# Optimization experiments

Hardware: AMD Instinct MI355X
Metric: run time of the kernel (lower is better)

Reference implementation:

```python
import jax, jax.numpy as jnp
import numpy as np

N_H, N_O, D = 5000, 15000, 1024
E_HH, E_OO, E_HO = 20000, 40000, 40000


def setup_inputs() -> dict:
    key = jax.random.key(0)
    ks = jax.random.split(key, 20)
    N = N_H + N_O
    w = lambda k, shp: jax.random.normal(k, shp, dtype=jnp.float32) * 0.02
    inp = {
        'n_f': jax.random.normal(ks[0], (N, D), dtype=jnp.float32),
        'src_hh': jax.random.randint(ks[1], (E_HH,), 0, N_H),
        'dst_hh': jax.random.randint(ks[2], (E_HH,), 0, N_H),
        'src_oo': jax.random.randint(ks[3], (E_OO,), 0, N_O) + N_H,
        'dst_oo': jax.random.randint(ks[4], (E_OO,), 0, N_O) + N_H,
        'src_ho': jax.random.randint(ks[5], (E_HO,), 0, N_H),
        'dst_ho': jax.random.randint(ks[6], (E_HO,), 0, N_O) + N_H,
        'W_hh': w(ks[7], (2 * D, D)), 'b_hh': jnp.zeros((D,), jnp.float32),
        'W_oo': w(ks[8], (2 * D, D)), 'b_oo': jnp.zeros((D,), jnp.float32),
        'W_ho': w(ks[9], (2 * D, D)), 'b_ho': jnp.zeros((D,), jnp.float32),
        'W_att': w(ks[10], (D, 1)), 'b_att': jnp.zeros((1,), jnp.float32),
        'W_hn': w(ks[11], (2 * D, D)), 'b_hn': jnp.zeros((D,), jnp.float32),
        'W_on': w(ks[12], (2 * D, D)), 'b_on': jnp.zeros((D,), jnp.float32),
    }
    return inp


def reference(n_f, src_hh, dst_hh, src_oo, dst_oo, src_ho, dst_ho,
              W_hh, b_hh, W_oo, b_oo, W_ho, b_ho, W_att, b_att,
              W_hn, b_hn, W_on, b_on):
    N = n_f.shape[0]

    def edge_mlp(src, dst, W, b):
        # gather -> concat -> Linear -> ReLU  (H_H/O_O/H_O EdgeApplyModule)
        feat = jnp.concatenate([n_f[src], n_f[dst]], axis=1)  # [E, 2D]
        return jax.nn.relu(feat @ W + b)                       # [E, D]

    e_f = jnp.concatenate([
        edge_mlp(src_hh, dst_hh, W_hh, b_hh),
        edge_mlp(src_oo, dst_oo, W_oo, b_oo),
        edge_mlp(src_ho, dst_ho, W_ho, b_ho),
    ], axis=0)                                                 # [E, D]
    src = jnp.concatenate([src_hh, src_oo, src_ho])
    dst = jnp.concatenate([dst_hh, dst_oo, dst_ho])

    # E_AttentionModule: per-edge scalar attention logit
    a = (e_f @ W_att + b_att)[:, 0]                            # [E]

    # update_all: per-destination softmax over incoming edges (mailbox softmax)
    seg_max = jax.ops.segment_max(a, dst, num_segments=N)
    seg_max = jnp.where(jnp.isfinite(seg_max), seg_max, 0.0)
    ex = jnp.exp(a - seg_max[dst])
    denom = jax.ops.segment_sum(ex, dst, num_segments=N)
    alpha = ex / jnp.where(denom[dst] == 0, 1.0, denom[dst])   # [E]
    z = jax.ops.segment_sum(alpha[:, None] * n_f[src], dst, num_segments=N)  # [N, D]

    # Node apply: concat(n_f, z_f) -> Linear -> ReLU, separate h/o MLPs
    new_h = jax.nn.relu(jnp.concatenate([n_f[:N_H], z[:N_H]], axis=1) @ W_hn + b_hn)
    new_o = jax.nn.relu(jnp.concatenate([n_f[N_H:], z[N_H:]], axis=1) @ W_on + b_on)
    return jnp.concatenate([new_h, new_o], axis=0)             # [N, D] new_n_f
```

## Files before the change

### kernel.cpp

```cpp
#include <hip/hip_runtime.h>

#define N_H   5000
#define N_O   15000
#define N_TOT 20000
#define DD    1024
#define E_HH  20000
#define E_OO  40000
#define E_HO  40000
#define E_TOT 100000

typedef unsigned short u16;
typedef unsigned int u32;
typedef __attribute__((ext_vector_type(8))) short short8;
typedef __attribute__((ext_vector_type(4))) float f32x4;
typedef const __attribute__((address_space(1))) u32 gas_u32;
typedef __attribute__((address_space(3))) u32 las_u32;

__device__ __forceinline__ float bf2f(u16 u) {
    union { unsigned int i; float f; } v; v.i = ((unsigned int)u) << 16; return v.f;
}
__device__ __forceinline__ u16 f2bf(float f) {
    union { float f; unsigned int i; } v; v.f = f;
    unsigned int u = v.i;
    return (u16)((u + 0x7FFFu + ((u >> 16) & 1u)) >> 16);
}

#define CAST_NB 10000
__global__ void cast_cat(const float* __restrict__ in, u16* __restrict__ out,
                         const int* __restrict__ shh, const int* __restrict__ dhh,
                         const int* __restrict__ soo, const int* __restrict__ doo,
                         const int* __restrict__ sho, const int* __restrict__ dho,
                         int* __restrict__ src_all, int* __restrict__ dst_all,
                         int* __restrict__ deg) {
    int b = blockIdx.x;
    if (b < CAST_NB) {
        size_t i = ((size_t)b * 256 + threadIdx.x) * 8;
        float4 a = *(const float4*)(in + i);
        float4 c = *(const float4*)(in + i + 4);
        u16 o[8] = {f2bf(a.x), f2bf(a.y), f2bf(a.z), f2bf(a.w),
                    f2bf(c.x), f2bf(c.y), f2bf(c.z), f2bf(c.w)};
        *(uint4*)(out + i) = *(const uint4*)o;
        return;
    }
    int e = (b - CAST_NB) * 256 + threadIdx.x;
    if (e >= E_TOT) return;
    int s, d;
    if (e < E_HH)              { s = shh[e];               d = dhh[e]; }
    else if (e < E_HH + E_OO)  { s = soo[e - E_HH];        d = doo[e - E_HH]; }
    else                       { s = sho[e - E_HH - E_OO]; d = dho[e - E_HH - E_OO]; }
    src_all[e] = s; dst_all[e] = d;
    atomicAdd(&deg[d], 1);
}

struct TW  { const float* W; u16* dT; u16* dB; int ld; };
struct TW5 { TW t[5]; };
__global__ void transpose_all(TW5 p) {
    __shared__ float tile[32][33];
    int z = blockIdx.z;
    TW tw = p.t[z >> 1];
    int half = z & 1;
    int bk = blockIdx.x, bn = blockIdx.y;
    int tx = threadIdx.x & 31, ty = threadIdx.x >> 5;
#pragma unroll
    for (int yy = 0; yy < 4; yy++) {
        int k = half * 1024 + bk * 32 + ty + yy * 8;
        int n = bn * 32 + tx;
        tile[ty + yy * 8][tx] = tw.W[(size_t)k * 1024 + n];
    }
    __syncthreads();
    u16* dst = half ? tw.dB : tw.dT;
#pragma unroll
    for (int yy = 0; yy < 4; yy++) {
        int n = bn * 32 + ty + yy * 8;
        int k = bk * 32 + tx;
        dst[(size_t)n * tw.ld + k] = f2bf(tile[tx][ty + yy * 8]);
    }
}

#define PROJ_NBM_H 40
#define PROJ_NBM_O 118
#define PROJ_NBN   24
__launch_bounds__(256)
__global__ void gemm_proj(const u16* __restrict__ Ah, const u16* __restrict__ Ao,
                          const u16* __restrict__ Bth, const u16* __restrict__ Bto,
                          u16* __restrict__ Ch, u16* __restrict__ Co) {
    __shared__ u16 smem[2][128][64];
    int bid = blockIdx.x;
    const u16* A; const u16* Bt; u16* C; int M;
    if (bid < PROJ_NBM_H * PROJ_NBN) { A = Ah; Bt = Bth; C = Ch; M = N_H; }
    else { bid -= PROJ_NBM_H * PROJ_NBN; A = Ao; Bt = Bto; C = Co; M = N_O; }
    int bm = bid / PROJ_NBN, bn = bid % PROJ_NBN;
    int t = threadIdx.x;
    int wave = t >> 6, lane = t & 63;
    int wr = wave >> 1, wc = wave & 1;
    int lm = lane & 15, q = lane >> 4;
    f32x4 acc[4][4] = {};
    int srow = lane >> 3;
    int scol = ((lane & 7) ^ srow) * 8;

    for (int k0 = 0; k0 < 1024; k0 += 64) {
#pragma unroll
        for (int it = 0; it < 4; it++) {
            int chunk = wave * 4 + it;
            int row = chunk * 8 + srow;
            int gr = bm * 128 + row; if (gr >= M) gr = M - 1;
            __builtin_amdgcn_global_load_lds((gas_u32*)(A + (size_t)gr * 1024 + k0 + scol),
                                             (las_u32*)&smem[0][chunk * 8][0], 16, 0, 0);
            __builtin_amdgcn_global_load_lds((gas_u32*)(Bt + (size_t)(bn * 128 + row) * 1024 + k0 + scol),
                                             (las_u32*)&smem[1][chunk * 8][0], 16, 0, 0);
        }
        __syncthreads();
#pragma unroll
        for (int ks = 0; ks < 64; ks += 32) {
            short8 af[4], bfr[4];
            int pc = (((ks >> 3) + q) ^ (lm & 7)) * 8;
#pragma unroll
            for (int i = 0; i < 4; i++)
                af[i] = *(const short8*)&smem[0][wr * 64 + i * 16 + lm][pc];
#pragma unroll
            for (int j = 0; j < 4; j++)
                bfr[j] = *(const short8*)&smem[1][wc * 64 + j * 16 + lm][pc];
#pragma unroll
            for (int i = 0; i < 4; i++)
#pragma unroll
                for (int j = 0; j < 4; j++)
                    acc[i][j] = __builtin_amdgcn_mfma_f32_16x16x32_bf16(af[i], bfr[j], acc[i][j], 0, 0, 0);
        }
        __syncthreads();
    }
    u16* sc = &smem[0][0][0];
#pragma unroll
    for (int i = 0; i < 4; i++)
#pragma unroll
        for (int j = 0; j < 4; j++)
#pragma unroll
            for (int r = 0; r < 4; r++)
                sc[(wr * 64 + i * 16 + q * 4 + r) * 128 + (wc * 64 + j * 16 + lm)] =
                    f2bf(acc[i][j][r]);
    __syncthreads();
#pragma unroll
    for (int it = 0; it < 8; it++) {
        int flat = it * 256 + t;
        int r = flat >> 4, cs = (flat & 15) * 8;
        int grow = bm * 128 + r;
        if (grow < M)
            *(uint4*)&C[(size_t)grow * 3072 + bn * 128 + cs] = *(const uint4*)&sc[r * 128 + cs];
    }
}

#define NODE_NBM_H 40
#define NODE_NBM_O 118
#define NODE_NBN   8
__launch_bounds__(256)
__global__ void gemm_node(const u16* __restrict__ nf_h, const u16* __restrict__ nf_o,
                          const u16* __restrict__ z_h, const u16* __restrict__ z_o,
                          const u16* __restrict__ Bthn, const u16* __restrict__ Bton,
                          const float* __restrict__ b_hn, const float* __restrict__ b_on,
                          float* __restrict__ out_h, float* __restrict__ out_o) {
    __shared__ u16 lA[128][64];
    __shared__ u16 lB[128][64];
    int bid = (blockIdx.x & 7) * ((NODE_NBM_H + NODE_NBM_O) * NODE_NBN / 8)
            + (blockIdx.x >> 3);
    const u16 *A0, *A1, *Bt; const float* bias; float* C; int M;
    if (bid < NODE_NBM_H * NODE_NBN) {
        A0 = nf_h; A1 = z_h; Bt = Bthn; bias = b_hn; C = out_h; M = N_H;
    } else {
        bid -= NODE_NBM_H * NODE_NBN;
        A0 = nf_o; A1 = z_o; Bt = Bton; bias = b_on; C = out_o; M = N_O;
    }
    int bm = bid / NODE_NBN, bn = bid % NODE_NBN;
    int t = threadIdx.x;
    int wave = t >> 6, lane = t & 63;
    int wr = wave >> 1, wc = wave & 1;
    int lm = lane & 15, q = lane >> 4;
    f32x4 acc[4][4] = {};
    int srow = lane >> 3;
    int scol = ((lane & 7) ^ srow) * 8;

    for (int half = 0; half < 2; half++) {
        const u16* Asrc = half ? A1 : A0;
        const u16* Bth = Bt + half * 1024;
        for (int k0 = 0; k0 < 1024; k0 += 64) {
#pragma unroll
            for (int it = 0; it < 4; it++) {
                int chunk = wave * 4 + it;
                int row = chunk * 8 + srow;
                int gr = bm * 128 + row; if (gr >= M) gr = M - 1;
                __builtin_amdgcn_global_load_lds((gas_u32*)(Asrc + (size_t)gr * 1024 + k0 + scol),
                                                 (las_u32*)&lA[chunk * 8][0], 16, 0, 0);
                __builtin_amdgcn_global_load_lds((gas_u32*)(Bth + (size_t)(bn * 128 + row) * 2048 + k0 + scol),
                                                 (las_u32*)&lB[chunk * 8][0], 16, 0, 0);
            }
            __syncthreads();
#pragma unroll
            for (int ks = 0; ks < 64; ks += 32) {
                short8 af[4], bfr[4];
                int pc = (((ks >> 3) + q) ^ (lm & 7)) * 8;
#pragma unroll
                for (int i = 0; i < 4; i++)
                    af[i] = *(const short8*)&lA[wr * 64 + i * 16 + lm][pc];
#pragma unroll
                for (int j = 0; j < 4; j++)
                    bfr[j] = *(const short8*)&lB[wc * 64 + j * 16 + lm][pc];
#pragma unroll
                for (int i = 0; i < 4; i++)
#pragma unroll
                    for (int j = 0; j < 4; j++)
                        acc[i][j] = __builtin_amdgcn_mfma_f32_16x16x32_bf16(af[i], bfr[j], acc[i][j], 0, 0, 0);
            }
            __syncthreads();
        }
    }
#pragma unroll
    for (int j = 0; j < 4; j++) {
        int col = bn * 128 + wc * 64 + j * 16 + lm;
        float bv = bias[col];
#pragma unroll
        for (int i = 0; i < 4; i++) {
            int row0 = bm * 128 + wr * 64 + i * 16 + q * 4;
#pragma unroll
            for (int r = 0; r < 4; r++) {
                int row = row0 + r;
                if (row < M)
                    C[(size_t)row * 1024 + col] = fmaxf(acc[i][j][r] + bv, 0.0f);
            }
        }
    }
}

__global__ void edge_att(const u16* __restrict__ proj_h, const u16* __restrict__ proj_o,
                         const float* __restrict__ b_hh, const float* __restrict__ b_oo,
                         const float* __restrict__ b_ho,
                         const float* __restrict__ W_att, const float* __restrict__ b_att,
                         const int* __restrict__ src_all, const int* __restrict__ dst_all,
                         float* __restrict__ a_out) {
    int wave = threadIdx.x >> 6, lane = threadIdx.x & 63;
    int e0 = blockIdx.x * 32 + wave * 8;
    const float* bsel = (e0 < E_HH) ? b_hh : (e0 < E_HH + E_OO ? b_oo : b_ho);
    float ww[16], bb[16];
#pragma unroll
    for (int i = 0; i < 16; i++) { ww[i] = W_att[lane * 16 + i]; bb[i] = bsel[lane * 16 + i]; }
    float batt = b_att[0];
#pragma unroll
    for (int k = 0; k < 8; k++) {
        int e = e0 + k;
        int s = src_all[e], d = dst_all[e];
        const u16 *u, *v;
        if (e < E_HH) {
            u = proj_h + (size_t)s * 3072;
            v = proj_h + (size_t)d * 3072 + 1024;
        } else if (e < E_HH + E_OO) {
            u = proj_o + (size_t)(s - N_H) * 3072;
            v = proj_o + (size_t)(d - N_H) * 3072 + 1024;
        } else {
            u = proj_h + (size_t)s * 3072 + 2048;
            v = proj_o + (size_t)(d - N_H) * 3072 + 2048;
        }
        int off = lane * 16;
        uint4 u0 = *(const uint4*)(u + off), u1 = *(const uint4*)(u + off + 8);
        uint4 v0 = *(const uint4*)(v + off), v1 = *(const uint4*)(v + off + 8);
        const u16* pu0 = (const u16*)&u0; const u16* pu1 = (const u16*)&u1;
        const u16* pv0 = (const u16*)&v0; const u16* pv1 = (const u16*)&v1;
        float acc = 0.f;
#pragma unroll
        for (int i = 0; i < 8; i++) {
            float tv = bf2f(pu0[i]) + bf2f(pv0[i]) + bb[i];
            acc += fmaxf(tv, 0.f) * ww[i];
        }
#pragma unroll
        for (int i = 0; i < 8; i++) {
            float tv = bf2f(pu1[i]) + bf2f(pv1[i]) + bb[8 + i];
            acc += fmaxf(tv, 0.f) * ww[8 + i];
        }
#pragma unroll
        for (int o = 32; o > 0; o >>= 1) acc += __shfl_down(acc, o);
        if (lane == 0) a_out[e] = acc + batt;
    }
}

__global__ void scan_deg(const int* __restrict__ deg, int* __restrict__ indptr) {
    __shared__ int sums[1024];
    int t = threadIdx.x;
    const int CH = 20;
    int beg = t * CH, end = beg + CH;
    if (end > N_TOT) end = N_TOT;
    if (beg > N_TOT) beg = N_TOT;
    int s = 0;
    for (int i = beg; i < end; i++) s += deg[i];
    sums[t] = s;
    __syncthreads();
    for (int off = 1; off < 1024; off <<= 1) {
        int v = sums[t];
        int add = (t >= off) ? sums[t - off] : 0;
        __syncthreads();
        sums[t] = v + add;
        __syncthreads();
    }
    int run = (t == 0) ? 0 : sums[t - 1];
    for (int i = beg; i < end; i++) { indptr[i] = run; run += deg[i]; }
    if (t == 1023) indptr[N_TOT] = sums[1023];
}

__global__ void fill_csr(const int* __restrict__ dst_all, const int* __restrict__ indptr,
                         int* __restrict__ cursor, int* __restrict__ edge_ids) {
    int e = blockIdx.x * 256 + threadIdx.x;
    if (e < E_TOT) {
        int d = dst_all[e];
        int pos = atomicAdd(&cursor[d], 1);
        edge_ids[indptr[d] + pos] = e;
    }
}

#define MAXDEG 1024
__global__ void soft_z(const float* __restrict__ a, const int* __restrict__ indptr,
                       const int* __restrict__ edge_ids, const int* __restrict__ src_all,
                       const u16* __restrict__ nf, u16* __restrict__ z) {
    __shared__ float s_a[MAXDEG];
    __shared__ int   s_src[MAXDEG];
    __shared__ float s_inv;
    int node = blockIdx.x;
    int t = threadIdx.x;
    int beg = indptr[node], end = indptr[node + 1];
    int deg = end - beg; if (deg > MAXDEG) deg = MAXDEG;
    if (t < 64) {
        float m = -1e30f;
        for (int i = t; i < deg; i += 64) {
            int eid = edge_ids[beg + i];
            float av = a[eid];
            s_a[i] = av;
            s_src[i] = src_all[eid];
            if (av > m) m = av;
        }
        for (int o = 32; o > 0; o >>= 1) m = fmaxf(m, __shfl_down(m, o));
        m = __shfl(m, 0);
        float ssum = 0.f;
        for (int i = t; i < deg; i += 64) {
            float ex = __expf(s_a[i] - m);
            s_a[i] = ex;
            ssum += ex;
        }
        for (int o = 32; o > 0; o >>= 1) ssum += __shfl_down(ssum, o);
        if (t == 0) s_inv = (ssum > 0.f) ? 1.0f / ssum : 0.f;
    }
    __syncthreads();
    float a0 = 0.f, a1 = 0.f, a2 = 0.f, a3 = 0.f;
    int base = t * 4;
    float inv = s_inv;
    for (int i = 0; i < deg; i++) {
        float al = s_a[i] * inv;
        const u16* row = nf + (size_t)s_src[i] * DD + base;
        uint2 p = *(const uint2*)row;
        const u16* pp = (const u16*)&p;
        a0 += al * bf2f(pp[0]); a1 += al * bf2f(pp[1]);
        a2 += al * bf2f(pp[2]); a3 += al * bf2f(pp[3]);
    }
    uint2 ov;
    u16* po = (u16*)&ov;
    po[0] = f2bf(a0); po[1] = f2bf(a1); po[2] = f2bf(a2); po[3] = f2bf(a3);
    *(uint2*)(z + (size_t)node * DD + base) = ov;
}

extern "C" void kernel_launch(void* const* d_in, const int* in_sizes, int n_in,
                              void* d_out, int out_size, void* d_ws, size_t ws_size,
                              hipStream_t stream) {
    const float* nf   = (const float*)d_in[0];
    const int* shh    = (const int*)d_in[1];
    const int* dhh    = (const int*)d_in[2];
    const int* soo    = (const int*)d_in[3];
    const int* doo    = (const int*)d_in[4];
    const int* sho    = (const int*)d_in[5];
    const int* dho    = (const int*)d_in[6];
    const float* W_hh = (const float*)d_in[7];
    const float* b_hh = (const float*)d_in[8];
    const float* W_oo = (const float*)d_in[9];
    const float* b_oo = (const float*)d_in[10];
    const float* W_ho = (const float*)d_in[11];
    const float* b_ho = (const float*)d_in[12];
    const float* W_att= (const float*)d_in[13];
    const float* b_att= (const float*)d_in[14];
    const float* W_hn = (const float*)d_in[15];
    const float* b_hn = (const float*)d_in[16];
    const float* W_on = (const float*)d_in[17];
    const float* b_on = (const float*)d_in[18];
    float* out = (float*)d_out;

    char* ws = (char*)d_ws;
    size_t off = 0;
    auto alloc = [&](size_t bytes) -> char* {
        char* p = ws + off;
        off += (bytes + 255) & ~(size_t)255;
        return p;
    };
    u16* nf_bf = (u16*)alloc((size_t)N_TOT * DD * 2);
    u16* Bt_h  = (u16*)alloc((size_t)3072 * 1024 * 2);
    u16* Bt_o  = (u16*)alloc((size_t)3072 * 1024 * 2);
    u16* Bt_hn = (u16*)alloc((size_t)1024 * 2048 * 2);
    u16* Bt_on = (u16*)alloc((size_t)1024 * 2048 * 2);
    u16* proj_h = (u16*)alloc((size_t)N_H * 3072 * 2);
    u16* proj_o = (u16*)alloc((size_t)N_O * 3072 * 2);
    u16* z_bf   = proj_h;
    float* a_log  = (float*)alloc(E_TOT * 4);
    int* src_all  = (int*)alloc(E_TOT * 4);
    int* dst_all  = (int*)alloc(E_TOT * 4);
    int* deg      = (int*)alloc(2 * N_TOT * 4);
    int* cursor   = deg + N_TOT;
    int* indptr   = (int*)alloc((N_TOT + 1) * 4);
    int* edge_ids = (int*)alloc(E_TOT * 4);
    (void)ws_size; (void)in_sizes; (void)n_in; (void)out_size;

    hipMemsetAsync(deg, 0, 2 * N_TOT * 4, stream);
    cast_cat<<<CAST_NB + (E_TOT + 255) / 256, 256, 0, stream>>>(
        nf, nf_bf, shh, dhh, soo, doo, sho, dho, src_all, dst_all, deg);

    TW5 tws;
    tws.t[0] = {W_hh, Bt_h,                       Bt_h + (size_t)1024 * 1024, 1024};
    tws.t[1] = {W_oo, Bt_o,                       Bt_o + (size_t)1024 * 1024, 1024};
    tws.t[2] = {W_ho, Bt_h + (size_t)2048 * 1024, Bt_o + (size_t)2048 * 1024, 1024};
    tws.t[3] = {W_hn, Bt_hn,                      Bt_hn + 1024,               2048};
    tws.t[4] = {W_on, Bt_on,                      Bt_on + 1024,               2048};
    transpose_all<<<dim3(32, 32, 10), 256, 0, stream>>>(tws);

    const u16* nf_bf_o = nf_bf + (size_t)N_H * DD;
    gemm_proj<<<(PROJ_NBM_H + PROJ_NBM_O) * PROJ_NBN, 256, 0, stream>>>(
        nf_bf, nf_bf_o, Bt_h, Bt_o, proj_h, proj_o);

    edge_att<<<E_TOT / 32, 256, 0, stream>>>(proj_h, proj_o, b_hh, b_oo, b_ho,
                                             W_att, b_att, src_all, dst_all, a_log);

    scan_deg<<<1, 1024, 0, stream>>>(deg, indptr);
    fill_csr<<<(E_TOT + 255) / 256, 256, 0, stream>>>(dst_all, indptr, cursor, edge_ids);

    soft_z<<<N_TOT, 256, 0, stream>>>(a_log, indptr, edge_ids, src_all, nf_bf, z_bf);

    gemm_node<<<(NODE_NBM_H + NODE_NBM_O) * NODE_NBN, 256, 0, stream>>>(
        nf_bf, nf_bf_o, z_bf, z_bf + (size_t)N_H * DD, Bt_hn, Bt_on,
        b_hn, b_on, out, out + (size_t)N_H * DD);
}
```

Baseline: 609.9 us.

## Fuse cast and weight transpose kernels, stage node GEMM epilogue, widen edge_att

```diff
diff --git a/kernel.cpp b/kernel.cpp
--- a/kernel.cpp
+++ b/kernel.cpp
@@ -26,12 +26,17 @@
 }
 
 #define CAST_NB 10000
-__global__ void cast_cat(const float* __restrict__ in, u16* __restrict__ out,
-                         const int* __restrict__ shh, const int* __restrict__ dhh,
-                         const int* __restrict__ soo, const int* __restrict__ doo,
-                         const int* __restrict__ sho, const int* __restrict__ dho,
-                         int* __restrict__ src_all, int* __restrict__ dst_all,
-                         int* __restrict__ deg) {
+#define CAT_NB  391
+#define TW_NB   10240
+struct TW  { const float* W; u16* dT; u16* dB; int ld; };
+struct TW5 { TW t[5]; };
+__global__ void cast_cat_tw(const float* __restrict__ in, u16* __restrict__ out,
+                            const int* __restrict__ shh, const int* __restrict__ dhh,
+                            const int* __restrict__ soo, const int* __restrict__ doo,
+                            const int* __restrict__ sho, const int* __restrict__ dho,
+                            int* __restrict__ src_all, int* __restrict__ dst_all,
+                            int* __restrict__ deg, TW5 p) {
+    __shared__ float tile[32][33];
     int b = blockIdx.x;
     if (b < CAST_NB) {
         size_t i = ((size_t)b * 256 + threadIdx.x) * 8;
@@ -42,24 +47,23 @@
         *(uint4*)(out + i) = *(const uint4*)o;
         return;
     }
-    int e = (b - CAST_NB) * 256 + threadIdx.x;
-    if (e >= E_TOT) return;
-    int s, d;
-    if (e < E_HH)              { s = shh[e];               d = dhh[e]; }
-    else if (e < E_HH + E_OO)  { s = soo[e - E_HH];        d = doo[e - E_HH]; }
-    else                       { s = sho[e - E_HH - E_OO]; d = dho[e - E_HH - E_OO]; }
-    src_all[e] = s; dst_all[e] = d;
-    atomicAdd(&deg[d], 1);
-}
-
-struct TW  { const float* W; u16* dT; u16* dB; int ld; };
-struct TW5 { TW t[5]; };
-__global__ void transpose_all(TW5 p) {
-    __shared__ float tile[32][33];
-    int z = blockIdx.z;
+    if (b < CAST_NB + CAT_NB) {
+        int e = (b - CAST_NB) * 256 + threadIdx.x;
+        if (e >= E_TOT) return;
+        int s, d;
+        if (e < E_HH)              { s = shh[e];               d = dhh[e]; }
+        else if (e < E_HH + E_OO)  { s = soo[e - E_HH];        d = doo[e - E_HH]; }
+        else                       { s = sho[e - E_HH - E_OO]; d = dho[e - E_HH - E_OO]; }
+        src_all[e] = s; dst_all[e] = d;
+        atomicAdd(&deg[d], 1);
+        return;
+    }
+    int tb = b - CAST_NB - CAT_NB;
+    int z = tb >> 10;
+    int rem = tb & 1023;
+    int bk = rem & 31, bn = rem >> 5;
     TW tw = p.t[z >> 1];
     int half = z & 1;
-    int bk = blockIdx.x, bn = blockIdx.y;
     int tx = threadIdx.x & 31, ty = threadIdx.x >> 5;
 #pragma unroll
     for (int yy = 0; yy < 4; yy++) {
@@ -157,8 +161,7 @@
                           const u16* __restrict__ Bthn, const u16* __restrict__ Bton,
                           const float* __restrict__ b_hn, const float* __restrict__ b_on,
                           float* __restrict__ out_h, float* __restrict__ out_o) {
-    __shared__ u16 lA[128][64];
-    __shared__ u16 lB[128][64];
+    __shared__ u16 smem[2][128][64];
     int bid = (blockIdx.x & 7) * ((NODE_NBM_H + NODE_NBM_O) * NODE_NBN / 8)
             + (blockIdx.x >> 3);
     const u16 *A0, *A1, *Bt; const float* bias; float* C; int M;
@@ -187,9 +190,9 @@
                 int row = chunk * 8 + srow;
                 int gr = bm * 128 + row; if (gr >= M) gr = M - 1;
                 __builtin_amdgcn_global_load_lds((gas_u32*)(Asrc + (size_t)gr * 1024 + k0 + scol),
-                                                 (las_u32*)&lA[chunk * 8][0], 16, 0, 0);
+                                                 (las_u32*)&smem[0][chunk * 8][0], 16, 0, 0);
                 __builtin_amdgcn_global_load_lds((gas_u32*)(Bth + (size_t)(bn * 128 + row) * 2048 + k0 + scol),
-                                                 (las_u32*)&lB[chunk * 8][0], 16, 0, 0);
+                                                 (las_u32*)&smem[1][chunk * 8][0], 16, 0, 0);
             }
             __syncthreads();
 #pragma unroll
@@ -198,10 +201,10 @@
                 int pc = (((ks >> 3) + q) ^ (lm & 7)) * 8;
 #pragma unroll
                 for (int i = 0; i < 4; i++)
-                    af[i] = *(const short8*)&lA[wr * 64 + i * 16 + lm][pc];
+                    af[i] = *(const short8*)&smem[0][wr * 64 + i * 16 + lm][pc];
 #pragma unroll
                 for (int j = 0; j < 4; j++)
-                    bfr[j] = *(const short8*)&lB[wc * 64 + j * 16 + lm][pc];
+                    bfr[j] = *(const short8*)&smem[1][wc * 64 + j * 16 + lm][pc];
 #pragma unroll
                 for (int i = 0; i < 4; i++)
 #pragma unroll
@@ -211,19 +214,32 @@
             __syncthreads();
         }
     }
-#pragma unroll
-    for (int j = 0; j < 4; j++) {
-        int col = bn * 128 + wc * 64 + j * 16 + lm;
-        float bv = bias[col];
-#pragma unroll
-        for (int i = 0; i < 4; i++) {
-            int row0 = bm * 128 + wr * 64 + i * 16 + q * 4;
-#pragma unroll
-            for (int r = 0; r < 4; r++) {
-                int row = row0 + r;
-                if (row < M)
-                    C[(size_t)row * 1024 + col] = fmaxf(acc[i][j][r] + bv, 0.0f);
+    float* sf = (float*)&smem[0][0][0];
+#pragma unroll
+    for (int p = 0; p < 2; p++) {
+        if (p) __syncthreads();
+        if (wr == p) {
+#pragma unroll
+            for (int j = 0; j < 4; j++) {
+                int col = wc * 64 + j * 16 + lm;
+                float bv = bias[bn * 128 + col];
+#pragma unroll
+                for (int i = 0; i < 4; i++)
+#pragma unroll
+                    for (int r = 0; r < 4; r++)
+                        sf[(i * 16 + q * 4 + r) * 128 + col] =
+                            fmaxf(acc[i][j][r] + bv, 0.0f);
             }
+        }
+        __syncthreads();
+#pragma unroll
+        for (int it = 0; it < 8; it++) {
+            int c = it * 256 + t;
+            int rl = c >> 5, k4 = c & 31;
+            int grow = bm * 128 + p * 64 + rl;
+            if (grow < M)
+                *(float4*)&C[(size_t)grow * 1024 + bn * 128 + k4 * 4] =
+                    *(const float4*)&sf[rl * 128 + k4 * 4];
         }
     }
 }
@@ -235,14 +251,14 @@
                          const int* __restrict__ src_all, const int* __restrict__ dst_all,
                          float* __restrict__ a_out) {
     int wave = threadIdx.x >> 6, lane = threadIdx.x & 63;
-    int e0 = blockIdx.x * 32 + wave * 8;
+    int e0 = blockIdx.x * 64 + wave * 16;
+    if (e0 >= E_TOT) return;
     const float* bsel = (e0 < E_HH) ? b_hh : (e0 < E_HH + E_OO ? b_oo : b_ho);
     float ww[16], bb[16];
 #pragma unroll
     for (int i = 0; i < 16; i++) { ww[i] = W_att[lane * 16 + i]; bb[i] = bsel[lane * 16 + i]; }
     float batt = b_att[0];
-#pragma unroll
-    for (int k = 0; k < 8; k++) {
+    for (int k = 0; k < 16; k++) {
         int e = e0 + k;
         int s = src_all[e], d = dst_all[e];
         const u16 *u, *v;
@@ -409,23 +425,21 @@
     (void)ws_size; (void)in_sizes; (void)n_in; (void)out_size;
 
     hipMemsetAsync(deg, 0, 2 * N_TOT * 4, stream);
-    cast_cat<<<CAST_NB + (E_TOT + 255) / 256, 256, 0, stream>>>(
-        nf, nf_bf, shh, dhh, soo, doo, sho, dho, src_all, dst_all, deg);
-
     TW5 tws;
     tws.t[0] = {W_hh, Bt_h,                       Bt_h + (size_t)1024 * 1024, 1024};
     tws.t[1] = {W_oo, Bt_o,                       Bt_o + (size_t)1024 * 1024, 1024};
     tws.t[2] = {W_ho, Bt_h + (size_t)2048 * 1024, Bt_o + (size_t)2048 * 1024, 1024};
     tws.t[3] = {W_hn, Bt_hn,                      Bt_hn + 1024,               2048};
     tws.t[4] = {W_on, Bt_on,                      Bt_on + 1024,               2048};
-    transpose_all<<<dim3(32, 32, 10), 256, 0, stream>>>(tws);
+    cast_cat_tw<<<CAST_NB + CAT_NB + TW_NB, 256, 0, stream>>>(
+        nf, nf_bf, shh, dhh, soo, doo, sho, dho, src_all, dst_all, deg, tws);
 
     const u16* nf_bf_o = nf_bf + (size_t)N_H * DD;
     gemm_proj<<<(PROJ_NBM_H + PROJ_NBM_O) * PROJ_NBN, 256, 0, stream>>>(
         nf_bf, nf_bf_o, Bt_h, Bt_o, proj_h, proj_o);
 
-    edge_att<<<E_TOT / 32, 256, 0, stream>>>(proj_h, proj_o, b_hh, b_oo, b_ho,
-                                             W_att, b_att, src_all, dst_all, a_log);
+    edge_att<<<(E_TOT + 63) / 64, 256, 0, stream>>>(proj_h, proj_o, b_hh, b_oo, b_ho,
+                                                    W_att, b_att, src_all, dst_all, a_log);
 
     scan_deg<<<1, 1024, 0, stream>>>(deg, indptr);
     fill_csr<<<(E_TOT + 255) / 256, 256, 0, stream>>>(dst_all, indptr, cursor, edge_ids);
```

Result: faster. 591.7 us (-3.0%).
